# Kernel optimization log

Hardware: AMD Instinct MI355X
Metric: run time of the kernel (lower is better)

Reference implementation:

```python
import jax, jax.numpy as jnp
import numpy as np

EPS_WN = 1e-6
EPS_BN = 1e-5

def wn_linear(x, W):
    # WeightNormlinear with scale=False, bias=False: y = (x W^T) / ||W_row||
    norm = jnp.sqrt(jnp.sum(W * W, axis=1) + EPS_WN)  # [out]
    return (x @ W.T) / norm

def hyper_weights(z, W0, W2, W3):
    # z: [N_O, N_I, E] -> conv weight [N_O*16, N_I*16, 3, 3], bias [N_O*16]
    N_O, N_I, E = z.shape
    bias = wn_linear(z.reshape(N_O, N_I * E), W0).reshape(-1)      # [N_O*16]
    w = wn_linear(z, W2).reshape(N_O, N_I, 16, E)                  # fc2
    w = wn_linear(w, W3)                                           # fc3 -> [N_O,N_I,16,16*9]
    w = w.reshape(N_O, N_I, 16, 16, 3, 3).transpose(0, 2, 1, 3, 4, 5)
    w = w.reshape(N_O * 16, N_I * 16, 3, 3)
    return jnp.sign(w), jnp.sign(bias)  # BinarizeWF forward

def conv3x3(x, w, stride):
    return jax.lax.conv_general_dilated(
        x, w, (stride, stride), ((1, 1), (1, 1)),
        dimension_numbers=('NCHW', 'OIHW', 'NCHW'))

def batchnorm(x, gamma, beta):
    # training-mode BN: biased batch statistics over (N,H,W)
    mean = jnp.mean(x, axis=(0, 2, 3), keepdims=True)
    var = jnp.var(x, axis=(0, 2, 3), keepdims=True)
    return gamma[None, :, None, None] * (x - mean) * jax.lax.rsqrt(var + EPS_BN) + beta[None, :, None, None]

def setup_inputs() -> dict:
    key = jax.random.key(0)
    ks = jax.random.split(key, 10)
    B, C, H, W = 16, 256, 56, 56
    E = 64
    NO = NI = C // 16
    def uni(k, shape, s):
        return jax.random.uniform(k, shape, jnp.float32, -s, s)
    stdv_z = 5.0 / np.sqrt(E)          # random_z init
    stdv0 = 4.0 / np.sqrt(E * NI)      # fc0: in = E*N_I
    stdv23 = 4.0 / np.sqrt(E)          # fc2/fc3: in = E
    return {
        'x': jax.random.normal(ks[0], (B, C, H, W), jnp.float32),
        'z1': uni(ks[1], (NO, NI, E), stdv_z),
        'W0_1': uni(ks[2], (16, E * NI), stdv0),
        'W2_1': uni(ks[3], (16 * E, E), stdv23),
        'W3_1': uni(ks[4], (16 * 9, E), stdv23),
        'gamma1': jnp.ones((C,), jnp.float32),
        'beta1': jnp.zeros((C,), jnp.float32),
        'z2': uni(ks[5], (NO, NO, E), stdv_z),
        'W0_2': uni(ks[6], (16, E * NO), stdv0),
        'W2_2': uni(ks[7], (16 * E, E), stdv23),
        'W3_2': uni(ks[8], (16 * 9, E), stdv23),
        'gamma2': jnp.ones((C,), jnp.float32),
        'beta2': jnp.zeros((C,), jnp.float32),
    }

def reference(x, z1, W0_1, W2_1, W3_1, gamma1, beta1,
              z2, W0_2, W2_2, W3_2, gamma2, beta2):
    residual = x
    # conv1 (stride=1): binarize activations (C != 3), hyper-generated binary weights
    w1, b1 = hyper_weights(z1, W0_1, W2_1, W3_1)
    out = conv3x3(jnp.sign(x), w1, 1) + b1[None, :, None, None]
    out = batchnorm(out, gamma1, beta1)
    # conv2
    w2, b2 = hyper_weights(z2, W0_2, W2_2, W3_2)
    out2 = conv3x3(jnp.sign(out), w2, 1) + b2[None, :, None, None]
    out2 = batchnorm(out2, gamma2, beta2)
    return out2 + residual
```

## Files before the change

kernel.cpp:

```cpp
#include <hip/hip_runtime.h>
#include <stdint.h>

typedef int v4i __attribute__((ext_vector_type(4)));
typedef int v16i __attribute__((ext_vector_type(16)));



__global__ void prep_kernel(unsigned long long* __restrict__ sums,
                            const float* __restrict__ z1, const float* __restrict__ W01,
                            const float* __restrict__ z2, const float* __restrict__ W02,
                            int* __restrict__ b1, int* __restrict__ b2) {
  const int tid = threadIdx.x;
  if (blockIdx.x == 32) {
    #pragma unroll
    for (int i = 0; i < 4; ++i) sums[i * 256 + tid] = 0ull;
    return;
  }
  __shared__ float zs[1024];
  const int sb = blockIdx.x;
  const int set = sb >> 4, o = sb & 15;
  const float* z = set ? z2 : z1;
  const float* W0 = set ? W02 : W01;
  int* bout = set ? b2 : b1;
  #pragma unroll
  for (int i = 0; i < 4; ++i) zs[i * 256 + tid] = z[(size_t)o * 1024 + i * 256 + tid];
  __syncthreads();
  const int j = tid >> 4, l = tid & 15;
  const float* wr = W0 + (size_t)j * 1024;
  double acc = 0.0;
  #pragma unroll 4
  for (int it = 0; it < 16; ++it) {
    float4 w4 = *(const float4*)&wr[it * 64 + l * 4];
    float4 z4 = *(const float4*)&zs[it * 64 + l * 4];
    acc += (double)w4.x * z4.x + (double)w4.y * z4.y + (double)w4.z * z4.z + (double)w4.w * z4.w;
  }
  #pragma unroll
  for (int m = 1; m < 16; m <<= 1) acc += __shfl_xor(acc, m, 64);
  if (l == 0) bout[o * 16 + j] = (acc > 0.0) ? 1 : ((acc < 0.0) ? -1 : 0);
}


__global__ __launch_bounds__(256, 2) void hyper_kernel(
    const float* __restrict__ z1, const float* __restrict__ W21,
    const float* __restrict__ W31, const float* __restrict__ z2,
    const float* __restrict__ W22, const float* __restrict__ W32,
    int8_t* __restrict__ Wb1, int8_t* __restrict__ Wb2) {
  __shared__ __align__(16) float Wt[16384];
  __shared__ __align__(16) float hbuf[1024];
  __shared__ __align__(16) float zsh[64];
  __shared__ __align__(16) int8_t pk[2304];
  const int tid = threadIdx.x;
  const int set = blockIdx.x >> 8;
  const int oi = blockIdx.x & 255;
  const float* z = set ? z2 : z1;
  const float* W2 = set ? W22 : W21;
  const float* W3 = set ? W32 : W31;
  int8_t* Wb = set ? Wb2 : Wb1;

  if (tid < 16) *(float4*)&zsh[tid * 4] = ((const float4*)(z + (size_t)oi * 64))[tid];
  __syncthreads();

  for (int c = 0; c < 4; ++c) {
    if (c) __syncthreads();
    const float4* src = (const float4*)W2 + c * 4096;
    #pragma unroll
    for (int i = 0; i < 16; ++i) {
      int G = i * 256 + tid;
      int row = G >> 4, g = G & 15;
      *(float4*)&Wt[row * 64 + ((g ^ (row & 15)) << 2)] = src[G];
    }
    __syncthreads();
    double ax = 0, ay = 0, az = 0, aw = 0;
    double nx = 0, ny = 0, nz = 0, nw = 0;
    #pragma unroll
    for (int it = 0; it < 16; ++it) {
      float4 w4 = *(const float4*)&Wt[tid * 64 + ((it ^ (tid & 15)) << 2)];
      float4 z4 = *(const float4*)&zsh[it * 4];
      ax += (double)w4.x * z4.x; ay += (double)w4.y * z4.y;
      az += (double)w4.z * z4.z; aw += (double)w4.w * z4.w;
      nx += (double)w4.x * w4.x; ny += (double)w4.y * w4.y;
      nz += (double)w4.z * w4.z; nw += (double)w4.w * w4.w;
    }
    double dot = (ax + ay) + (az + aw);
    double ss = (nx + ny) + (nz + nw);
    hbuf[c * 256 + tid] = (float)(dot / sqrt(ss + 1e-6));
  }
  __syncthreads();

  {
    const float4* src = (const float4*)W3;
    #pragma unroll
    for (int i = 0; i < 9; ++i) {
      int G = i * 256 + tid;
      int row = G >> 4, g = G & 15;
      *(float4*)&Wt[row * 64 + ((g ^ (row & 15)) << 2)] = src[G];
    }
  }
  __syncthreads();

  {
    const int q = tid >> 4, sub = tid & 15;
    #pragma unroll
    for (int k = 0; k < 9; ++k) {
      int jj = sub + (k << 4);
      double ax = 0, ay = 0, az = 0, aw = 0;
      #pragma unroll
      for (int it = 0; it < 16; ++it) {
        float4 w4 = *(const float4*)&Wt[jj * 64 + ((it ^ sub) << 2)];
        float4 h4 = *(const float4*)&hbuf[q * 64 + it * 4];
        ax += (double)w4.x * h4.x; ay += (double)w4.y * h4.y;
        az += (double)w4.z * h4.z; aw += (double)w4.w * h4.w;
      }
      double acc = (ax + ay) + (az + aw);
      int8_t sgn = (acc > 0.0) ? (int8_t)1 : ((acc < 0.0) ? (int8_t)(-1) : (int8_t)0);
      int tp = jj / 9, tap = jj - tp * 9;
      pk[tap * 256 + q * 16 + tp] = sgn;
    }
  }
  __syncthreads();

  if (tid < 144) {
    const int tap = tid >> 4, qq = tid & 15;
    const int o = oi >> 4, ii = oi & 15;
    const int chunk = ((tap << 2) + (ii >> 2)) * 2 + ((ii >> 1) & 1);
    v4i val = *(const v4i*)&pk[tap * 256 + qq * 16];
    *(v4i*)(Wb + (size_t)chunk * 8192 + (size_t)(o * 16 + qq) * 32 + ((ii & 1) << 4)) = val;
  }
}


__global__ void signx_kernel(const float* __restrict__ x, int8_t* __restrict__ Sp) {
  const int tid = threadIdx.x;
  const int h = blockIdx.x, b = blockIdx.y;
  int8_t* rowp = Sp + ((size_t)b * 58 + h) * 58 * 256;
  if (h == 0 || h == 57) {
    #pragma unroll
    for (int i = 0; i < 4; ++i) {
      int idx = i * 256 + tid;
      if (idx < 928) *(v4i*)(rowp + (size_t)idx * 16) = (v4i){0, 0, 0, 0};
    }
    return;
  }
  __shared__ int8_t t[56 * 256];
  const float* xb = x + (size_t)b * 802816 + (size_t)(h - 1) * 56;
  for (int i = 0; i < 56; ++i) {
    int flat = i * 256 + tid;
    int c = flat / 56, w = flat - c * 56;
    float v = xb[(size_t)c * 3136 + w];
    t[w * 256 + (c ^ ((w & 31) << 3))] = (v > 0.f) ? 1 : ((v < 0.f) ? -1 : 0);
  }
  if (tid < 32) {
    int col = tid >> 4;
    *(v4i*)(rowp + (col ? 57 * 256 : 0) + (tid & 15) * 16) = (v4i){0, 0, 0, 0};
  }
  __syncthreads();
  int8_t* dst = rowp + 256;
  for (int i = 0; i < 7; ++i) {
    int f8 = i * 256 + tid;
    int w = f8 >> 5, c0 = (f8 & 31) << 3;
    uint2 v = *(const uint2*)&t[w * 256 + (c0 ^ ((w & 31) << 3))];
    *(uint2*)(dst + (size_t)w * 256 + c0) = v;
  }
}


template <int MODE>
__global__ __launch_bounds__(256, 2) void conv_kernel(
    const int8_t* __restrict__ Sp, const int16_t* __restrict__ rawin,
    const float* __restrict__ par, const int8_t* __restrict__ WbP,
    const int* __restrict__ bias, int16_t* __restrict__ raw,
    unsigned long long* __restrict__ sums)
{
  __shared__ __align__(16) int8_t lds[59392];
  const int tid = threadIdx.x;
  const int lane = tid & 63;
  const int b = blockIdx.y;
  const int H0 = blockIdx.x << 1;

  const int n = lane & 31, kg = lane >> 5;
  const int cogrp = tid >> 6;

  const int8_t* Abase = WbP + (size_t)((cogrp << 6) + n) * 32 + (kg << 4);
  v4i Ar[3][2][2];
  #pragma unroll
  for (int c2 = 0; c2 < 2; ++c2)
    #pragma unroll
    for (int a = 0; a < 2; ++a) {
      Ar[0][c2][a] = *(const v4i*)(Abase + (size_t)(0 * 2 + c2) * 8192 + a * 1024);
      Ar[1][c2][a] = *(const v4i*)(Abase + (size_t)(1 * 2 + c2) * 8192 + a * 1024);
    }

  if (MODE == 0) {
    const int8_t* SpB = Sp + ((size_t)b * 58 + H0) * 58 * 256;
    #pragma unroll
    for (int ph = 0; ph < 2; ++ph) {
      v4i tmp[8];
      #pragma unroll
      for (int it = 0; it < 8; ++it) {
        int G = (ph * 8 + it) * 256 + tid;
        if (G < 3712) {
          int pp = G >> 4, gl = G & 15;
          int wp = pp % 58;
          tmp[it] = *(const v4i*)(SpB + pp * 256 + ((gl ^ (wp & 7)) << 4));
        }
      }
      #pragma unroll
      for (int it = 0; it < 8; ++it) {
        int G = (ph * 8 + it) * 256 + tid;
        if (G < 3712) *(v4i*)(lds + (G << 4)) = tmp[it];
      }
    }
  } else {
    const int gsrc = tid & 15;
    const int ppt = tid >> 4;
    float thr[16]; int sf[16];
    const float* thrp = par + 768;
    const int* sfp = (const int*)(par + 1024);
    #pragma unroll
    for (int j = 0; j < 16; ++j) { thr[j] = thrp[gsrc * 16 + j]; sf[j] = sfp[gsrc * 16 + j]; }
    #pragma unroll
    for (int it = 0; it < 15; ++it) {
      int pp = it * 16 + ppt;
      if (pp < 232) {
        int prow = pp / 58, pcol = pp - prow * 58;
        int ir = H0 + prow - 1, ic = pcol - 1;
        v4i outv = (v4i){0, 0, 0, 0};
        if (ir >= 0 && ir <= 55 && ic >= 0 && ic <= 55) {
          const int16_t* src = rawin + ((size_t)(b * 3136 + ir * 56 + ic)) * 256 + gsrc * 16;
          v4i lo = *(const v4i*)src;
          v4i hi = *(const v4i*)(src + 8);
          #pragma unroll
          for (int j = 0; j < 16; ++j) {
            int wd = (j < 8) ? lo[(j >> 1) & 3] : hi[(j >> 1) & 3];
            int v = (j & 1) ? (wd >> 16) : (int)(short)wd;
            float fv = (float)v;
            int bj = (fv > thr[j]) ? sf[j] : ((fv < thr[j]) ? -sf[j] : 0);
            outv[j >> 2] |= (bj & 0xff) << ((j & 3) << 3);
          }
        }
        *(v4i*)(lds + ((pp << 4) + (gsrc ^ (pcol & 7))) * 16) = outv;
      }
    }
  }

  int pixoff[4], wcol[4];
  #pragma unroll
  for (int f = 0; f < 4; ++f) {
    int px = (f << 5) + n;
    if (px > 111) px = 111;
    int hh = px / 56, ww = px - hh * 56;
    pixoff[f] = hh * 58 + ww;
    wcol[f] = ww;
  }

  v16i acc[4][2];
  #pragma unroll
  for (int f = 0; f < 4; ++f)
    #pragma unroll
    for (int a = 0; a < 2; ++a)
      #pragma unroll
      for (int e = 0; e < 16; ++e) acc[f][a][e] = 0;

  __syncthreads();

  #pragma unroll
  for (int ks = 0; ks < 36; ++ks) {
    if (ks + 2 < 36) {
      const int bn = (ks + 2) % 3;
      #pragma unroll
      for (int c2 = 0; c2 < 2; ++c2)
        #pragma unroll
        for (int a = 0; a < 2; ++a)
          Ar[bn][c2][a] = *(const v4i*)(Abase + (size_t)((ks + 2) * 2 + c2) * 8192 + a * 1024);
    }
    const int cur = ks % 3;
    const int tap = ks >> 2, c64 = ks & 3;
    const int r = tap / 3, s = tap - 3 * (tap / 3);
    #pragma unroll
    for (int c2 = 0; c2 < 2; ++c2) {
      v4i Af0 = Ar[cur][c2][0], Af1 = Ar[cur][c2][1];
      #pragma unroll
      for (int f = 0; f < 4; ++f) {
        const int gb = (c64 << 2) + (c2 << 1) + kg;
        v4i Bf = *(const v4i*)(lds + ((pixoff[f] + r * 58 + s) << 8)
                               + ((gb ^ ((wcol[f] + s) & 7)) << 4));
        acc[f][0] = __builtin_amdgcn_mfma_i32_32x32x32_i8(Af0, Bf, acc[f][0], 0, 0, 0);
        acc[f][1] = __builtin_amdgcn_mfma_i32_32x32x32_i8(Af1, Bf, acc[f][1], 0, 0, 0);
      }
    }
  }

  __syncthreads();
  #pragma unroll
  for (int f = 0; f < 4; ++f) {
    int px = (f << 5) + n;
    if (px < 112) {
      #pragma unroll
      for (int a = 0; a < 2; ++a) {
        #pragma unroll
        for (int q = 0; q < 4; ++q) {
          int co = (cogrp << 6) + (a << 5) + (q << 3) + (kg << 2);
          v4i bi = *(const v4i*)(bias + co);
          short4 o;
          o.x = (short)(acc[f][a][q * 4 + 0] + bi.x);
          o.y = (short)(acc[f][a][q * 4 + 1] + bi.y);
          o.z = (short)(acc[f][a][q * 4 + 2] + bi.z);
          o.w = (short)(acc[f][a][q * 4 + 3] + bi.w);
          int g = co >> 3;
          *(short4*)(lds + px * 512 + ((g ^ (px & 31)) << 4) + (kg << 3)) = o;
        }
      }
    }
  }
  __syncthreads();
  const int pbase = b * 3136 + blockIdx.x * 112;
  const int gg = tid & 31;
  int s8[8], q8[8];
  #pragma unroll
  for (int j = 0; j < 8; ++j) { s8[j] = 0; q8[j] = 0; }
  #pragma unroll
  for (int i = 0; i < 14; ++i) {
    int rrow = i * 8 + (tid >> 5);
    v4i val = *(const v4i*)(lds + rrow * 512 + ((gg ^ (rrow & 31)) << 4));
    *(v4i*)(raw + (size_t)(pbase + rrow) * 256 + gg * 8) = val;
    #pragma unroll
    for (int j = 0; j < 8; ++j) {
      int wd = val[j >> 1];
      int v = (j & 1) ? (wd >> 16) : (int)(short)wd;
      s8[j] += v; q8[j] += v * v;
    }
  }
  __syncthreads();
  int* red = (int*)lds;
  #pragma unroll
  for (int j = 0; j < 8; ++j) { red[tid * 8 + j] = s8[j]; red[2048 + tid * 8 + j] = q8[j]; }
  __syncthreads();
  {
    const int ch = tid;
    const int own = ch >> 3, sub = ch & 7;
    long long S = 0, Q = 0;
    #pragma unroll
    for (int jj = 0; jj < 8; ++jj) {
      int t2 = own + 32 * jj;
      S += red[t2 * 8 + sub];
      Q += red[2048 + t2 * 8 + sub];
    }
    atomicAdd(&sums[ch], (unsigned long long)S);
    atomicAdd(&sums[256 + ch], (unsigned long long)Q);
  }
}


__global__ void finalize_kernel(const unsigned long long* __restrict__ sums,
                                const float* __restrict__ gamma, const float* __restrict__ beta,
                                float* __restrict__ par) {
  const int c = threadIdx.x;
  double S = (double)(long long)sums[c];
  double Q = (double)(long long)sums[256 + c];
  double mean = S / 50176.0;
  double var = Q / 50176.0 - mean * mean;
  double istd = 1.0 / sqrt(var + 1e-5);
  double A = (double)gamma[c] * istd;
  float Af = (float)A;
  par[c] = (float)mean;
  par[256 + c] = Af;
  par[512 + c] = beta[c];
  float thr; int sf;
  if (Af > 0.f)      { thr = (float)(mean - (double)beta[c] / A); sf = 1; }
  else if (Af < 0.f) { thr = (float)(mean - (double)beta[c] / A); sf = -1; }
  else               { thr = -1e30f; sf = (beta[c] > 0.f) ? 1 : ((beta[c] < 0.f) ? -1 : 0); }
  par[768 + c] = thr;
  ((int*)par)[1024 + c] = sf;
}


__global__ void final_kernel(const int16_t* __restrict__ raw2, const float* __restrict__ par,
                             const float* __restrict__ x, float* __restrict__ out) {
  __shared__ float t[256 * 57];
  const int tid = threadIdx.x;
  const int h = blockIdx.x, b = blockIdx.y;
  const int rowp = b * 3136 + h * 56;
  for (int i = 0; i < 7; ++i) {
    int f8 = i * 256 + tid;
    int px = f8 >> 5, c0 = (f8 & 31) << 3;
    float m[8], A[8], bb[8];
    *(float4*)&m[0]  = *(const float4*)&par[c0];
    *(float4*)&m[4]  = *(const float4*)&par[c0 + 4];
    *(float4*)&A[0]  = *(const float4*)&par[256 + c0];
    *(float4*)&A[4]  = *(const float4*)&par[256 + c0 + 4];
    *(float4*)&bb[0] = *(const float4*)&par[512 + c0];
    *(float4*)&bb[4] = *(const float4*)&par[512 + c0 + 4];
    v4i vv = *(const v4i*)(raw2 + (size_t)(rowp + px) * 256 + c0);
    #pragma unroll
    for (int j = 0; j < 8; ++j) {
      int wd = vv[j >> 1];
      int v = (j & 1) ? (wd >> 16) : (int)(short)wd;
      t[(c0 + j) * 57 + px] = ((float)v - m[j]) * A[j] + bb[j];
    }
  }
  __syncthreads();
  const float* xb = x + (size_t)b * 802816 + (size_t)h * 56;
  float* ob = out + (size_t)b * 802816 + (size_t)h * 56;
  for (int i = 0; i < 16; ++i) {
    int idx = i * 256 + tid;
    int c = idx >> 4, wq = idx & 15;
    if (wq < 14) {
      int w0 = wq * 4;
      float4 xv = *(const float4*)(xb + (size_t)c * 3136 + w0);
      float4 o;
      o.x = t[c * 57 + w0 + 0] + xv.x;
      o.y = t[c * 57 + w0 + 1] + xv.y;
      o.z = t[c * 57 + w0 + 2] + xv.z;
      o.w = t[c * 57 + w0 + 3] + xv.w;
      *(float4*)(ob + (size_t)c * 3136 + w0) = o;
    }
  }
}


extern "C" void kernel_launch(void* const* d_in, const int* in_sizes, int n_in,
                              void* d_out, int out_size, void* d_ws, size_t ws_size,
                              hipStream_t stream) {
  const float* x      = (const float*)d_in[0];
  const float* z1     = (const float*)d_in[1];
  const float* W0_1   = (const float*)d_in[2];
  const float* W2_1   = (const float*)d_in[3];
  const float* W3_1   = (const float*)d_in[4];
  const float* gamma1 = (const float*)d_in[5];
  const float* beta1  = (const float*)d_in[6];
  const float* z2     = (const float*)d_in[7];
  const float* W0_2   = (const float*)d_in[8];
  const float* W2_2   = (const float*)d_in[9];
  const float* W3_2   = (const float*)d_in[10];
  const float* gamma2 = (const float*)d_in[11];
  const float* beta2  = (const float*)d_in[12];
  float* out = (float*)d_out;

  char* ws = (char*)d_ws;
  size_t off = 0;
  auto alloc = [&](size_t sz) -> void* {
    void* p = ws + off;
    off += (sz + 255) & ~(size_t)255;
    return p;
  };
  int8_t* Sp1   = (int8_t*)alloc(13778944);
  int16_t* raw1 = (int16_t*)alloc(25690112);
  int16_t* raw2 = (int16_t*)alloc(25690112);
  int8_t* Wb1   = (int8_t*)alloc(589824);
  int8_t* Wb2   = (int8_t*)alloc(589824);
  int* b1       = (int*)alloc(1024);
  int* b2       = (int*)alloc(1024);
  unsigned long long* sums = (unsigned long long*)alloc(8192);
  float* par1   = (float*)alloc(5120);
  float* par2   = (float*)alloc(5120);
  if (ws_size < off) return;

  prep_kernel<<<33, 256, 0, stream>>>(sums, z1, W0_1, z2, W0_2, b1, b2);
  hyper_kernel<<<512, 256, 0, stream>>>(z1, W2_1, W3_1, z2, W2_2, W3_2, Wb1, Wb2);
  signx_kernel<<<dim3(58, 16), 256, 0, stream>>>(x, Sp1);
  conv_kernel<0><<<dim3(28, 16), 256, 0, stream>>>(Sp1, nullptr, nullptr, Wb1, b1, raw1, sums);
  finalize_kernel<<<1, 256, 0, stream>>>(sums, gamma1, beta1, par1);
  conv_kernel<1><<<dim3(28, 16), 256, 0, stream>>>(nullptr, raw1, par1, Wb2, b2, raw2, sums + 512);
  finalize_kernel<<<1, 256, 0, stream>>>(sums + 512, gamma2, beta2, par2);
  final_kernel<<<dim3(56, 16), 256, 0, stream>>>(raw2, par2, x, out);
}
```

Measured before the change: 188.5 us.

## Shrink conv tile to one output row and fold prep into hyper kernel

Each conv block now computes one output row (56 pixels) instead of two, so the grid doubles to 56x16. This shrinks LDS use and halves the accumulator count, which allows launch bounds of 3 blocks per CU for more occupancy and better wave coverage. The cost is that each block re-stages 3 input rows to produce only 1, raising halo overhead and weight-register reloads per output. Separately, the prep (bias and sums-zeroing) kernel is merged into hyper_kernel as 33 extra blocks, which removes one launch.

```diff
diff --git a/kernel.cpp b/kernel.cpp
--- a/kernel.cpp
+++ b/kernel.cpp
@@ -4,52 +4,52 @@
 typedef int v4i __attribute__((ext_vector_type(4)));
 typedef int v16i __attribute__((ext_vector_type(16)));
 
-
-
-__global__ void prep_kernel(unsigned long long* __restrict__ sums,
-                            const float* __restrict__ z1, const float* __restrict__ W01,
-                            const float* __restrict__ z2, const float* __restrict__ W02,
-                            int* __restrict__ b1, int* __restrict__ b2) {
-  const int tid = threadIdx.x;
-  if (blockIdx.x == 32) {
-    #pragma unroll
-    for (int i = 0; i < 4; ++i) sums[i * 256 + tid] = 0ull;
-    return;
-  }
-  __shared__ float zs[1024];
-  const int sb = blockIdx.x;
-  const int set = sb >> 4, o = sb & 15;
-  const float* z = set ? z2 : z1;
-  const float* W0 = set ? W02 : W01;
-  int* bout = set ? b2 : b1;
-  #pragma unroll
-  for (int i = 0; i < 4; ++i) zs[i * 256 + tid] = z[(size_t)o * 1024 + i * 256 + tid];
-  __syncthreads();
-  const int j = tid >> 4, l = tid & 15;
-  const float* wr = W0 + (size_t)j * 1024;
-  double acc = 0.0;
-  #pragma unroll 4
-  for (int it = 0; it < 16; ++it) {
-    float4 w4 = *(const float4*)&wr[it * 64 + l * 4];
-    float4 z4 = *(const float4*)&zs[it * 64 + l * 4];
-    acc += (double)w4.x * z4.x + (double)w4.y * z4.y + (double)w4.z * z4.z + (double)w4.w * z4.w;
-  }
-  #pragma unroll
-  for (int m = 1; m < 16; m <<= 1) acc += __shfl_xor(acc, m, 64);
-  if (l == 0) bout[o * 16 + j] = (acc > 0.0) ? 1 : ((acc < 0.0) ? -1 : 0);
-}
 
 
 __global__ __launch_bounds__(256, 2) void hyper_kernel(
     const float* __restrict__ z1, const float* __restrict__ W21,
     const float* __restrict__ W31, const float* __restrict__ z2,
     const float* __restrict__ W22, const float* __restrict__ W32,
-    int8_t* __restrict__ Wb1, int8_t* __restrict__ Wb2) {
+    int8_t* __restrict__ Wb1, int8_t* __restrict__ Wb2,
+    const float* __restrict__ W01, const float* __restrict__ W02,
+    int* __restrict__ b1, int* __restrict__ b2,
+    unsigned long long* __restrict__ sums) {
   __shared__ __align__(16) float Wt[16384];
   __shared__ __align__(16) float hbuf[1024];
   __shared__ __align__(16) float zsh[64];
   __shared__ __align__(16) int8_t pk[2304];
   const int tid = threadIdx.x;
+
+  if (blockIdx.x >= 512) {
+    const int pb = blockIdx.x - 512;
+    if (pb == 32) {
+      #pragma unroll
+      for (int i = 0; i < 4; ++i) sums[i * 256 + tid] = 0ull;
+      return;
+    }
+    float* zs = Wt;
+    const int set = pb >> 4, o = pb & 15;
+    const float* z = set ? z2 : z1;
+    const float* W0 = set ? W02 : W01;
+    int* bout = set ? b2 : b1;
+    #pragma unroll
+    for (int i = 0; i < 4; ++i) zs[i * 256 + tid] = z[(size_t)o * 1024 + i * 256 + tid];
+    __syncthreads();
+    const int j = tid >> 4, l = tid & 15;
+    const float* wr = W0 + (size_t)j * 1024;
+    double acc = 0.0;
+    #pragma unroll 4
+    for (int it = 0; it < 16; ++it) {
+      float4 w4 = *(const float4*)&wr[it * 64 + l * 4];
+      float4 z4 = *(const float4*)&zs[it * 64 + l * 4];
+      acc += (double)w4.x * z4.x + (double)w4.y * z4.y + (double)w4.z * z4.z + (double)w4.w * z4.w;
+    }
+    #pragma unroll
+    for (int m = 1; m < 16; m <<= 1) acc += __shfl_xor(acc, m, 64);
+    if (l == 0) bout[o * 16 + j] = (acc > 0.0) ? 1 : ((acc < 0.0) ? -1 : 0);
+    return;
+  }
+
   const int set = blockIdx.x >> 8;
   const int oi = blockIdx.x & 255;
   const float* z = set ? z2 : z1;
@@ -165,17 +165,17 @@
 
 
 template <int MODE>
-__global__ __launch_bounds__(256, 2) void conv_kernel(
+__global__ __launch_bounds__(256, 3) void conv_kernel(
     const int8_t* __restrict__ Sp, const int16_t* __restrict__ rawin,
     const float* __restrict__ par, const int8_t* __restrict__ WbP,
     const int* __restrict__ bias, int16_t* __restrict__ raw,
     unsigned long long* __restrict__ sums)
 {
-  __shared__ __align__(16) int8_t lds[59392];
+  __shared__ __align__(16) int8_t lds[44544];
   const int tid = threadIdx.x;
   const int lane = tid & 63;
   const int b = blockIdx.y;
-  const int H0 = blockIdx.x << 1;
+  const int H = blockIdx.x;
 
   const int n = lane & 31, kg = lane >> 5;
   const int cogrp = tid >> 6;
@@ -191,23 +191,23 @@
     }
 
   if (MODE == 0) {
-    const int8_t* SpB = Sp + ((size_t)b * 58 + H0) * 58 * 256;
-    #pragma unroll
-    for (int ph = 0; ph < 2; ++ph) {
-      v4i tmp[8];
-      #pragma unroll
-      for (int it = 0; it < 8; ++it) {
-        int G = (ph * 8 + it) * 256 + tid;
-        if (G < 3712) {
+    const int8_t* SpB = Sp + ((size_t)b * 58 + H) * 58 * 256;
+    #pragma unroll
+    for (int ph = 0; ph < 3; ++ph) {
+      v4i tmp[4];
+      #pragma unroll
+      for (int it = 0; it < 4; ++it) {
+        int G = (ph * 4 + it) * 256 + tid;
+        if (G < 2784) {
           int pp = G >> 4, gl = G & 15;
           int wp = pp % 58;
           tmp[it] = *(const v4i*)(SpB + pp * 256 + ((gl ^ (wp & 7)) << 4));
         }
       }
       #pragma unroll
-      for (int it = 0; it < 8; ++it) {
-        int G = (ph * 8 + it) * 256 + tid;
-        if (G < 3712) *(v4i*)(lds + (G << 4)) = tmp[it];
+      for (int it = 0; it < 4; ++it) {
+        int G = (ph * 4 + it) * 256 + tid;
+        if (G < 2784) *(v4i*)(lds + (G << 4)) = tmp[it];
       }
     }
   } else {
@@ -219,11 +219,11 @@
     #pragma unroll
     for (int j = 0; j < 16; ++j) { thr[j] = thrp[gsrc * 16 + j]; sf[j] = sfp[gsrc * 16 + j]; }
     #pragma unroll
-    for (int it = 0; it < 15; ++it) {
+    for (int it = 0; it < 11; ++it) {
       int pp = it * 16 + ppt;
-      if (pp < 232) {
+      if (pp < 174) {
         int prow = pp / 58, pcol = pp - prow * 58;
-        int ir = H0 + prow - 1, ic = pcol - 1;
+        int ir = H + prow - 1, ic = pcol - 1;
         v4i outv = (v4i){0, 0, 0, 0};
         if (ir >= 0 && ir <= 55 && ic >= 0 && ic <= 55) {
           const int16_t* src = rawin + ((size_t)(b * 3136 + ir * 56 + ic)) * 256 + gsrc * 16;
@@ -243,19 +243,17 @@
     }
   }
 
-  int pixoff[4], wcol[4];
-  #pragma unroll
-  for (int f = 0; f < 4; ++f) {
+  int wcol[2];
+  #pragma unroll
+  for (int f = 0; f < 2; ++f) {
     int px = (f << 5) + n;
-    if (px > 111) px = 111;
-    int hh = px / 56, ww = px - hh * 56;
-    pixoff[f] = hh * 58 + ww;
-    wcol[f] = ww;
-  }
-
-  v16i acc[4][2];
-  #pragma unroll
-  for (int f = 0; f < 4; ++f)
+    if (px > 55) px = 55;
+    wcol[f] = px;
+  }
+
+  v16i acc[2][2];
+  #pragma unroll
+  for (int f = 0; f < 2; ++f)
     #pragma unroll
     for (int a = 0; a < 2; ++a)
       #pragma unroll
@@ -280,10 +278,10 @@
     for (int c2 = 0; c2 < 2; ++c2) {
       v4i Af0 = Ar[cur][c2][0], Af1 = Ar[cur][c2][1];
       #pragma unroll
-      for (int f = 0; f < 4; ++f) {
+      for (int f = 0; f < 2; ++f) {
         const int gb = (c64 << 2) + (c2 << 1) + kg;
-        v4i Bf = *(const v4i*)(lds + ((pixoff[f] + r * 58 + s) << 8)
-                               + ((gb ^ ((wcol[f] + s) & 7)) << 4));
+        const int col = wcol[f] + s;
+        v4i Bf = *(const v4i*)(lds + ((r * 58 + col) << 8) + ((gb ^ (col & 7)) << 4));
         acc[f][0] = __builtin_amdgcn_mfma_i32_32x32x32_i8(Af0, Bf, acc[f][0], 0, 0, 0);
         acc[f][1] = __builtin_amdgcn_mfma_i32_32x32x32_i8(Af1, Bf, acc[f][1], 0, 0, 0);
       }
@@ -292,9 +290,9 @@
 
   __syncthreads();
   #pragma unroll
-  for (int f = 0; f < 4; ++f) {
+  for (int f = 0; f < 2; ++f) {
     int px = (f << 5) + n;
-    if (px < 112) {
+    if (px < 56) {
       #pragma unroll
       for (int a = 0; a < 2; ++a) {
         #pragma unroll
@@ -313,13 +311,13 @@
     }
   }
   __syncthreads();
-  const int pbase = b * 3136 + blockIdx.x * 112;
+  const int pbase = b * 3136 + H * 56;
   const int gg = tid & 31;
   int s8[8], q8[8];
   #pragma unroll
   for (int j = 0; j < 8; ++j) { s8[j] = 0; q8[j] = 0; }
   #pragma unroll
-  for (int i = 0; i < 14; ++i) {
+  for (int i = 0; i < 7; ++i) {
     int rrow = i * 8 + (tid >> 5);
     v4i val = *(const v4i*)(lds + rrow * 512 + ((gg ^ (rrow & 31)) << 4));
     *(v4i*)(raw + (size_t)(pbase + rrow) * 256 + gg * 8) = val;
@@ -455,12 +453,12 @@
   float* par2   = (float*)alloc(5120);
   if (ws_size < off) return;
 
-  prep_kernel<<<33, 256, 0, stream>>>(sums, z1, W0_1, z2, W0_2, b1, b2);
-  hyper_kernel<<<512, 256, 0, stream>>>(z1, W2_1, W3_1, z2, W2_2, W3_2, Wb1, Wb2);
+  hyper_kernel<<<545, 256, 0, stream>>>(z1, W2_1, W3_1, z2, W2_2, W3_2, Wb1, Wb2,
+                                        W0_1, W0_2, b1, b2, sums);
   signx_kernel<<<dim3(58, 16), 256, 0, stream>>>(x, Sp1);
-  conv_kernel<0><<<dim3(28, 16), 256, 0, stream>>>(Sp1, nullptr, nullptr, Wb1, b1, raw1, sums);
+  conv_kernel<0><<<dim3(56, 16), 256, 0, stream>>>(Sp1, nullptr, nullptr, Wb1, b1, raw1, sums);
   finalize_kernel<<<1, 256, 0, stream>>>(sums, gamma1, beta1, par1);
-  conv_kernel<1><<<dim3(28, 16), 256, 0, stream>>>(nullptr, raw1, par1, Wb2, b2, raw2, sums + 512);
+  conv_kernel<1><<<dim3(56, 16), 256, 0, stream>>>(nullptr, raw1, par1, Wb2, b2, raw2, sums + 512);
   finalize_kernel<<<1, 256, 0, stream>>>(sums + 512, gamma2, beta2, par2);
   final_kernel<<<dim3(56, 16), 256, 0, stream>>>(raw2, par2, x, out);
 }
```

Measured after the change: 217.5 us. 15.4% more time.

## Merge prep into hyper kernel and remap block indices for XCD locality

Applied to the files above, without the earlier changes.

Folds the bias/sum-reset prep work into the hyper kernel as 33 extra blocks, removing one kernel launch. It also remaps the flattened block index in the signx, conv and final kernels so that consecutive blocks on the same XCD (blocks are dealt round-robin across 8 XCDs) process contiguous rows and batches. The aim is better L2 locality per XCD and less launch overhead. The cost is a little index arithmetic and a larger shared-memory footprint for the former prep blocks.

```diff
diff --git a/kernel.cpp b/kernel.cpp
--- a/kernel.cpp
+++ b/kernel.cpp
@@ -4,52 +4,52 @@
 typedef int v4i __attribute__((ext_vector_type(4)));
 typedef int v16i __attribute__((ext_vector_type(16)));
 
-
-
-__global__ void prep_kernel(unsigned long long* __restrict__ sums,
-                            const float* __restrict__ z1, const float* __restrict__ W01,
-                            const float* __restrict__ z2, const float* __restrict__ W02,
-                            int* __restrict__ b1, int* __restrict__ b2) {
-  const int tid = threadIdx.x;
-  if (blockIdx.x == 32) {
-    #pragma unroll
-    for (int i = 0; i < 4; ++i) sums[i * 256 + tid] = 0ull;
-    return;
-  }
-  __shared__ float zs[1024];
-  const int sb = blockIdx.x;
-  const int set = sb >> 4, o = sb & 15;
-  const float* z = set ? z2 : z1;
-  const float* W0 = set ? W02 : W01;
-  int* bout = set ? b2 : b1;
-  #pragma unroll
-  for (int i = 0; i < 4; ++i) zs[i * 256 + tid] = z[(size_t)o * 1024 + i * 256 + tid];
-  __syncthreads();
-  const int j = tid >> 4, l = tid & 15;
-  const float* wr = W0 + (size_t)j * 1024;
-  double acc = 0.0;
-  #pragma unroll 4
-  for (int it = 0; it < 16; ++it) {
-    float4 w4 = *(const float4*)&wr[it * 64 + l * 4];
-    float4 z4 = *(const float4*)&zs[it * 64 + l * 4];
-    acc += (double)w4.x * z4.x + (double)w4.y * z4.y + (double)w4.z * z4.z + (double)w4.w * z4.w;
-  }
-  #pragma unroll
-  for (int m = 1; m < 16; m <<= 1) acc += __shfl_xor(acc, m, 64);
-  if (l == 0) bout[o * 16 + j] = (acc > 0.0) ? 1 : ((acc < 0.0) ? -1 : 0);
-}
 
 
 __global__ __launch_bounds__(256, 2) void hyper_kernel(
     const float* __restrict__ z1, const float* __restrict__ W21,
     const float* __restrict__ W31, const float* __restrict__ z2,
     const float* __restrict__ W22, const float* __restrict__ W32,
-    int8_t* __restrict__ Wb1, int8_t* __restrict__ Wb2) {
+    int8_t* __restrict__ Wb1, int8_t* __restrict__ Wb2,
+    const float* __restrict__ W01, const float* __restrict__ W02,
+    int* __restrict__ b1, int* __restrict__ b2,
+    unsigned long long* __restrict__ sums) {
   __shared__ __align__(16) float Wt[16384];
   __shared__ __align__(16) float hbuf[1024];
   __shared__ __align__(16) float zsh[64];
   __shared__ __align__(16) int8_t pk[2304];
   const int tid = threadIdx.x;
+
+  if (blockIdx.x >= 512) {
+    const int pb = blockIdx.x - 512;
+    if (pb == 32) {
+      #pragma unroll
+      for (int i = 0; i < 4; ++i) sums[i * 256 + tid] = 0ull;
+      return;
+    }
+    float* zs = Wt;
+    const int set = pb >> 4, o = pb & 15;
+    const float* z = set ? z2 : z1;
+    const float* W0 = set ? W02 : W01;
+    int* bout = set ? b2 : b1;
+    #pragma unroll
+    for (int i = 0; i < 4; ++i) zs[i * 256 + tid] = z[(size_t)o * 1024 + i * 256 + tid];
+    __syncthreads();
+    const int j = tid >> 4, l = tid & 15;
+    const float* wr = W0 + (size_t)j * 1024;
+    double acc = 0.0;
+    #pragma unroll 4
+    for (int it = 0; it < 16; ++it) {
+      float4 w4 = *(const float4*)&wr[it * 64 + l * 4];
+      float4 z4 = *(const float4*)&zs[it * 64 + l * 4];
+      acc += (double)w4.x * z4.x + (double)w4.y * z4.y + (double)w4.z * z4.z + (double)w4.w * z4.w;
+    }
+    #pragma unroll
+    for (int m = 1; m < 16; m <<= 1) acc += __shfl_xor(acc, m, 64);
+    if (l == 0) bout[o * 16 + j] = (acc > 0.0) ? 1 : ((acc < 0.0) ? -1 : 0);
+    return;
+  }
+
   const int set = blockIdx.x >> 8;
   const int oi = blockIdx.x & 255;
   const float* z = set ? z2 : z1;
@@ -131,7 +131,9 @@
 
 __global__ void signx_kernel(const float* __restrict__ x, int8_t* __restrict__ Sp) {
   const int tid = threadIdx.x;
-  const int h = blockIdx.x, b = blockIdx.y;
+  const int f = blockIdx.x + 58 * blockIdx.y;
+  const int orig = (f & 7) * 116 + (f >> 3);
+  const int b = orig / 58, h = orig % 58;
   int8_t* rowp = Sp + ((size_t)b * 58 + h) * 58 * 256;
   if (h == 0 || h == 57) {
     #pragma unroll
@@ -174,8 +176,10 @@
   __shared__ __align__(16) int8_t lds[59392];
   const int tid = threadIdx.x;
   const int lane = tid & 63;
-  const int b = blockIdx.y;
-  const int H0 = blockIdx.x << 1;
+  const int f0 = blockIdx.x + 28 * blockIdx.y;
+  const int orig = (f0 & 7) * 56 + (f0 >> 3);
+  const int b = orig / 28, bx = orig % 28;
+  const int H0 = bx << 1;
 
   const int n = lane & 31, kg = lane >> 5;
   const int cogrp = tid >> 6;
@@ -313,7 +317,7 @@
     }
   }
   __syncthreads();
-  const int pbase = b * 3136 + blockIdx.x * 112;
+  const int pbase = b * 3136 + bx * 112;
   const int gg = tid & 31;
   int s8[8], q8[8];
   #pragma unroll
@@ -378,7 +382,9 @@
                              const float* __restrict__ x, float* __restrict__ out) {
   __shared__ float t[256 * 57];
   const int tid = threadIdx.x;
-  const int h = blockIdx.x, b = blockIdx.y;
+  const int f0 = blockIdx.x + 56 * blockIdx.y;
+  const int orig = (f0 & 7) * 112 + (f0 >> 3);
+  const int b = orig / 56, h = orig % 56;
   const int rowp = b * 3136 + h * 56;
   for (int i = 0; i < 7; ++i) {
     int f8 = i * 256 + tid;
@@ -455,8 +461,8 @@
   float* par2   = (float*)alloc(5120);
   if (ws_size < off) return;
 
-  prep_kernel<<<33, 256, 0, stream>>>(sums, z1, W0_1, z2, W0_2, b1, b2);
-  hyper_kernel<<<512, 256, 0, stream>>>(z1, W2_1, W3_1, z2, W2_2, W3_2, Wb1, Wb2);
+  hyper_kernel<<<545, 256, 0, stream>>>(z1, W2_1, W3_1, z2, W2_2, W3_2, Wb1, Wb2,
+                                        W0_1, W0_2, b1, b2, sums);
   signx_kernel<<<dim3(58, 16), 256, 0, stream>>>(x, Sp1);
   conv_kernel<0><<<dim3(28, 16), 256, 0, stream>>>(Sp1, nullptr, nullptr, Wb1, b1, raw1, sums);
   finalize_kernel<<<1, 256, 0, stream>>>(sums, gamma1, beta1, par1);
```

Result: faster. 175.1 us (-7.1%).
